# Kernel tuning notes

Hardware: AMD Instinct MI355X
Metric: run time of the kernel (lower is better)

Reference implementation:

```python
import jax, jax.numpy as jnp
import numpy as np

N, B, NPG, DEG, F = 16384, 128, 128, 8, 128
E = N * DEG
H1, C1, H2, C2, H3, C3 = 3, 128, 2, 64, 2, 32
D = H1 * C1 + H2 * C2 + C3  # 544
K = 30
ND = 2048
LAMDA = 0.8


def _gatv2(x, src, dst, Wl, Wr, att, b, h, c, concat):
    n = x.shape[0]
    xl = (x @ Wl).reshape(n, h, c)
    xr = (x @ Wr).reshape(n, h, c)
    e = jax.nn.leaky_relu(xl[src] + xr[dst], 0.2)           # [E+N, h, c]
    logit = jnp.einsum('ehc,hc->eh', e, att)
    m = jax.lax.stop_gradient(jax.ops.segment_max(logit, dst, num_segments=n))
    a = jnp.exp(logit - m[dst])
    z = jax.ops.segment_sum(a, dst, num_segments=n)
    a = a / z[dst]
    out = jax.ops.segment_sum(xl[src] * a[:, :, None], dst, num_segments=n)
    out = out.reshape(n, h * c) if concat else out.mean(axis=1)
    return out + b


def _bn(x, g, b):
    m = x.mean(0)
    v = ((x - m) ** 2).mean(0)
    return (x - m) * jax.lax.rsqrt(v + 1e-5) * g + b


def _neighbor(emb, adj, W, b, idx):
    h = emb @ W + b
    A = adj + jnp.eye(adj.shape[0], dtype=adj.dtype)
    d = jax.lax.rsqrt(A.sum(axis=1))
    h = (1.0 - LAMDA) * h + LAMDA * ((d[:, None] * A * d[None, :]) @ h)
    v = h[idx]
    return v / jnp.clip(jnp.linalg.norm(v, axis=1, keepdims=True), 1e-12)


def setup_inputs():
    key = jax.random.key(0)
    it = iter(jax.random.split(key, 48))
    def nrm(shape, s=0.05):
        return jax.random.normal(next(it), shape, jnp.float32) * s
    src = jnp.repeat(jnp.arange(N, dtype=jnp.int32), DEG)
    dst = (src // NPG) * NPG + jax.random.randint(next(it), (E,), 0, NPG, dtype=jnp.int32)
    batch = jnp.arange(N, dtype=jnp.int32) // NPG
    return dict(
        x=jax.random.normal(next(it), (N, F), jnp.float32),
        edge_src=src, edge_dst=dst, batch=batch,
        pairs1=jax.random.randint(next(it), (B,), 0, ND, dtype=jnp.int32),
        pairs2=jax.random.randint(next(it), (B,), 0, ND, dtype=jnp.int32),
        drug_adj=(jax.random.uniform(next(it), (ND, ND)) < 0.01).astype(jnp.float32),
        drug_emb=jax.random.normal(next(it), (ND, ND), jnp.float32) * 0.1,
        dis_adj=(jax.random.uniform(next(it), (ND, ND)) < 0.01).astype(jnp.float32),
        dis_emb=jax.random.normal(next(it), (ND, ND), jnp.float32) * 0.1,
        Wde=nrm((ND, 32)), bde=jnp.zeros((32,), jnp.float32),
        Wse=nrm((ND, 32)), bse=jnp.zeros((32,), jnp.float32),
        W1l=nrm((F, H1 * C1)), W1r=nrm((F, H1 * C1)), att1=nrm((H1, C1)), b1=jnp.zeros((H1 * C1,), jnp.float32),
        W2l=nrm((H1 * C1, H2 * C2)), W2r=nrm((H1 * C1, H2 * C2)), att2=nrm((H2, C2)), b2=jnp.zeros((H2 * C2,), jnp.float32),
        W3l=nrm((H2 * C2, H3 * C3)), W3r=nrm((H2 * C2, H3 * C3)), att3=nrm((H3, C3)), b3=jnp.zeros((C3,), jnp.float32),
        g1=jnp.ones((H1 * C1,), jnp.float32), be1=jnp.zeros((H1 * C1,), jnp.float32),
        g2=jnp.ones((H2 * C2,), jnp.float32), be2=jnp.zeros((H2 * C2,), jnp.float32),
        Ws=nrm((D, K)), bs=jnp.zeros((K,), jnp.float32),
        Wg=nrm((D, D)), bg=jnp.zeros((D,), jnp.float32),
        Wl1=nrm((D * K + 64, 128)), bl1=jnp.zeros((128,), jnp.float32),
        Wl2=nrm((128, 1)), bl2=jnp.zeros((1,), jnp.float32),
    )


def _forward(x, drug_adj, drug_emb, dis_adj, dis_emb, Wde, bde, Wse, bse,
             W1l, W1r, att1, b1, W2l, W2r, att2, b2, W3l, W3r, att3, b3,
             g1, be1, g2, be2, Ws, bs, Wg, bg, Wl1, bl1, Wl2, bl2,
             edge_src, edge_dst, batch, pairs1, pairs2):
    loop = jnp.arange(N, dtype=edge_src.dtype)  # GATv2 self loops
    src = jnp.concatenate([edge_src, loop])
    dst = jnp.concatenate([edge_dst, loop])
    x1 = _bn(jax.nn.relu(_gatv2(x, src, dst, W1l, W1r, att1, b1, H1, C1, True)), g1, be1)
    x2 = _bn(jax.nn.relu(_gatv2(x1, src, dst, W2l, W2r, att2, b2, H2, C2, True)), g2, be2)
    x3 = _gatv2(x2, src, dst, W3l, W3r, att3, b3, H3, C3, False)
    xc = jnp.concatenate([x1, x2, x3], axis=1)              # [N, D]
    xd = xc.reshape(B, NPG, D)                              # to_dense_batch (equal graphs)
    adj = jnp.zeros((B, NPG, NPG), xc.dtype).at[
        batch[edge_src], edge_src % NPG, edge_dst % NPG].add(1.0)
    s = jax.nn.softmax(xd @ Ws + bs, axis=-1)               # [B, NPG, K]
    xp = jnp.einsum('bnk,bnd->bkd', s, xd)                  # pooled features
    ap = jnp.einsum('bnk,bnm,bml->bkl', s, adj, s)          # pooled adjacency
    ap = ap.at[:, jnp.arange(K), jnp.arange(K)].set(1.0)    # DenseGCNConv add_loop
    dg = jax.lax.rsqrt(jnp.clip(ap.sum(-1), 1.0))
    apn = dg[:, :, None] * ap * dg[:, None, :]
    xg = jax.nn.relu(jnp.einsum('bkl,bld->bkd', apn, xp @ Wg) + bg)
    de = _neighbor(drug_emb, drug_adj, Wde, bde, pairs1)    # [B, 32]
    se = _neighbor(dis_emb, dis_adj, Wse, bse, pairs2)      # [B, 32]
    g = jnp.concatenate([de, xg.reshape(B, K * D), se], axis=-1)
    h = jax.nn.relu(g @ Wl1 + bl1)
    return (h @ Wl2 + bl2)[:, 0]


def reference(x, edge_src, edge_dst, batch, pairs1, pairs2, drug_adj, drug_emb, dis_adj, dis_emb,
              Wde, bde, Wse, bse, W1l, W1r, att1, b1, W2l, W2r, att2, b2, W3l, W3r, att3, b3,
              g1, be1, g2, be2, Ws, bs, Wg, bg, Wl1, bl1, Wl2, bl2):
    return _forward(x, drug_adj, drug_emb, dis_adj, dis_emb, Wde, bde, Wse, bse,
                    W1l, W1r, att1, b1, W2l, W2r, att2, b2, W3l, W3r, att3, b3,
                    g1, be1, g2, be2, Ws, bs, Wg, bg, Wl1, bl1, Wl2, bl2,
                    edge_src, edge_dst, batch, pairs1, pairs2)
```

## Files before the change

kernel.cpp:

```cpp
#include <hip/hip_runtime.h>
#include <math.h>

#define CDIV(a,b) (((a)+(b)-1)/(b))
#define HMIN(a,b) ((a)<(b)?(a):(b))
#define MAXD 48

typedef __attribute__((ext_vector_type(8))) short bf16x8;
typedef __attribute__((ext_vector_type(4))) float f32x4;

static __device__ inline short f2bf(float x){
  unsigned u = __float_as_uint(x);
  unsigned r = (u + 0x7fffu + ((u >> 16) & 1u)) >> 16;
  return (short)r;
}
static __device__ inline float bf2f(short s){
  return __uint_as_float(((unsigned)(unsigned short)s) << 16);
}

__global__ __launch_bounds__(256)
void transpose_bf16(const float* __restrict__ B, int K, int N, short* __restrict__ Bt)
{
  __shared__ float t[32][33];
  int k0 = blockIdx.x*32, n0 = blockIdx.y*32;
  int c = threadIdx.x & 31, r8 = threadIdx.x >> 5;
  for (int rr = r8; rr < 32; rr += 8) {
    int k = k0+rr, n = n0+c;
    t[rr][c] = (k < K && n < N) ? B[(size_t)k*N + n] : 0.f;
  }
  __syncthreads();
  for (int rr = r8; rr < 32; rr += 8) {
    int n = n0+rr, k = k0+c;
    if (n < N && k < K) Bt[(size_t)n*K + k] = f2bf(t[c][rr]);
  }
}

__global__ __launch_bounds__(256)
void gemm_mfma(const float* __restrict__ A, int lda,
               const short* __restrict__ Bt,
               float* __restrict__ C, int ldc,
               int M, int N, int K,
               const float* __restrict__ bias, int relu, int ksplit)
{
  __shared__ short As[128][40];
  __shared__ short Bs[128][40];
  const int k0 = blockIdx.z * ksplit;
  const int k1 = HMIN(k0 + ksplit, K);
  C += (size_t)blockIdx.z * (size_t)M * ldc;
  const int bm = blockIdx.x * 128, bn = blockIdx.y * 128;
  const int tid = threadIdx.x;
  const int sr = tid >> 1;
  const int sk = (tid & 1) * 16;
  const int wave = tid >> 6;
  const int wr = (wave >> 1) * 64, wc = (wave & 1) * 64;
  const int lane = tid & 63;
  const int lrow = lane & 15, lk = (lane >> 4) * 8;

  f32x4 acc[4][4];
  #pragma unroll
  for (int i=0;i<4;i++)
    #pragma unroll
    for (int j=0;j<4;j++) acc[i][j] = (f32x4){0.f,0.f,0.f,0.f};

  const bool bok = (bn + sr) < N;
  for (int kb = k0; kb < k1; kb += 32) {
    __syncthreads();
    {
      const float* ap = A + (size_t)(bm + sr)*lda + kb + sk;
      float4 v0 = *(const float4*)(ap+0);
      float4 v1 = *(const float4*)(ap+4);
      float4 v2 = *(const float4*)(ap+8);
      float4 v3 = *(const float4*)(ap+12);
      bf16x8 w0, w1;
      w0[0]=f2bf(v0.x); w0[1]=f2bf(v0.y); w0[2]=f2bf(v0.z); w0[3]=f2bf(v0.w);
      w0[4]=f2bf(v1.x); w0[5]=f2bf(v1.y); w0[6]=f2bf(v1.z); w0[7]=f2bf(v1.w);
      w1[0]=f2bf(v2.x); w1[1]=f2bf(v2.y); w1[2]=f2bf(v2.z); w1[3]=f2bf(v2.w);
      w1[4]=f2bf(v3.x); w1[5]=f2bf(v3.y); w1[6]=f2bf(v3.z); w1[7]=f2bf(v3.w);
      *(bf16x8*)&As[sr][sk]   = w0;
      *(bf16x8*)&As[sr][sk+8] = w1;
    }
    {
      bf16x8 u0 = (bf16x8){0,0,0,0,0,0,0,0}, u1 = u0;
      if (bok) {
        const short* bp = Bt + (size_t)(bn + sr)*K + kb + sk;
        u0 = *(const bf16x8*)(bp);
        u1 = *(const bf16x8*)(bp+8);
      }
      *(bf16x8*)&Bs[sr][sk]   = u0;
      *(bf16x8*)&Bs[sr][sk+8] = u1;
    }
    __syncthreads();
    bf16x8 af[4], bfr[4];
    #pragma unroll
    for (int f=0;f<4;f++) af[f]  = *(const bf16x8*)&As[wr + f*16 + lrow][lk];
    #pragma unroll
    for (int f=0;f<4;f++) bfr[f] = *(const bf16x8*)&Bs[wc + f*16 + lrow][lk];
    #pragma unroll
    for (int i=0;i<4;i++)
      #pragma unroll
      for (int j=0;j<4;j++)
        acc[i][j] = __builtin_amdgcn_mfma_f32_16x16x32_bf16(af[i], bfr[j], acc[i][j], 0, 0, 0);
  }
  const int erow = (lane >> 4) * 4;
  const int ecol = lane & 15;
  #pragma unroll
  for (int j=0;j<4;j++) {
    int gcol = bn + wc + j*16 + ecol;
    if (gcol >= N) continue;
    float bv = bias ? bias[gcol] : 0.f;
    #pragma unroll
    for (int i=0;i<4;i++) {
      int grow = bm + wr + i*16 + erow;
      #pragma unroll
      for (int r=0;r<4;r++) {
        float v = acc[i][j][r] + bv;
        if (relu) v = fmaxf(v, 0.f);
        C[(size_t)(grow + r)*ldc + gcol] = v;
      }
    }
  }
}

__global__ __launch_bounds__(256)
void skinny_gemm32(const float* __restrict__ A, int lda,
                   const float* __restrict__ B,
                   float* __restrict__ Cp, int M, int ksplit)
{
  const int m0 = blockIdx.x * 32;
  const int k0 = blockIdx.z * ksplit;
  __shared__ float As[32][68];
  __shared__ float Bs[64][36];
  float acc[4] = {0.f,0.f,0.f,0.f};
  const int r  = threadIdx.x >> 3;
  const int cg = (threadIdx.x & 7) * 4;
  for (int kb = k0; kb < k0 + ksplit; kb += 64) {
    {
      int rr = threadIdx.x >> 3, ko = (threadIdx.x & 7)*8;
      const float* ap = &A[(size_t)(m0+rr)*lda + kb + ko];
      *(float4*)&As[rr][ko]   = *(const float4*)ap;
      *(float4*)&As[rr][ko+4] = *(const float4*)(ap+4);
      int br = threadIdx.x >> 2, co = (threadIdx.x & 3)*8;
      const float* bp = &B[(size_t)(kb+br)*32 + co];
      *(float4*)&Bs[br][co]   = *(const float4*)bp;
      *(float4*)&Bs[br][co+4] = *(const float4*)(bp+4);
    }
    __syncthreads();
    #pragma unroll
    for (int kk=0; kk<64; kk+=4) {
      float4 a4 = *(const float4*)&As[r][kk];
      float4 b0 = *(const float4*)&Bs[kk  ][cg];
      float4 b1 = *(const float4*)&Bs[kk+1][cg];
      float4 b2 = *(const float4*)&Bs[kk+2][cg];
      float4 b3 = *(const float4*)&Bs[kk+3][cg];
      acc[0] += a4.x*b0.x + a4.y*b1.x + a4.z*b2.x + a4.w*b3.x;
      acc[1] += a4.x*b0.y + a4.y*b1.y + a4.z*b2.y + a4.w*b3.y;
      acc[2] += a4.x*b0.z + a4.y*b1.z + a4.z*b2.z + a4.w*b3.z;
      acc[3] += a4.x*b0.w + a4.y*b1.w + a4.z*b2.w + a4.w*b3.w;
    }
    __syncthreads();
  }
  float* cp = Cp + ((size_t)blockIdx.z*M + m0 + r)*32 + cg;
  *(float4*)cp = make_float4(acc[0],acc[1],acc[2],acc[3]);
}

__global__ void build_adj(const int* __restrict__ src, const int* __restrict__ dst,
                          int E, float* __restrict__ adj)
{
  int e = blockIdx.x*blockDim.x + threadIdx.x;
  if (e >= E) return;
  int s = src[e], d = dst[e];
  int g = s >> 7;
  atomicAdd(&adj[((size_t)g*128 + (s & 127))*128 + (d & 127)], 1.0f);
}

__global__ __launch_bounds__(1024)
void build_nbr(const int* __restrict__ dst, int epg, int shift,
               int* __restrict__ nbr, int* __restrict__ deg)
{
  __shared__ short ld[1024];
  const int g = blockIdx.x;
  for (int i = threadIdx.x; i < epg; i += 1024) ld[i] = (short)(dst[g*epg + i] & 127);
  __syncthreads();
  const int d   = threadIdx.x >> 3;
  const int seg = threadIdx.x & 7;
  const int spe = epg >> 3;
  const int i0 = seg*spe, i1 = i0 + spe;
  int cnt = 0;
  for (int i = i0; i < i1; ++i) cnt += (ld[i] == (short)d) ? 1 : 0;
  int pre = cnt;
  #pragma unroll
  for (int off=1; off<8; off<<=1) {
    int v = __shfl_up(pre, off, 8);
    if (seg >= off) pre += v;
  }
  const int base  = pre - cnt;
  const int total = __shfl(pre, 7, 8);
  if (seg == 7) deg[g*128 + d] = HMIN(total, MAXD);
  const int lbase = (g*128 + d)*MAXD;
  int w = base;
  for (int i = i0; i < i1; ++i) {
    if (ld[i] == (short)d) {
      if (w < MAXD) nbr[lbase + w] = i >> shift;
      ++w;
    }
  }
}

template<int C, int NL>
__global__ __launch_bounds__(512)
void gat_attn_sp(const float* __restrict__ XL, const float* __restrict__ XR, int ldx,
                 const float* __restrict__ att,
                 const int* __restrict__ nbr, const int* __restrict__ deg,
                 const float* __restrict__ bias, int bias_per_head,
                 float* __restrict__ out, int ldo)
{
  constexpr int SPAN = C / NL;
  constexpr int NG = 512 / NL;
  constexpr int PADC = C + 8;
  __shared__ short xls[128][PADC];
  __shared__ float A_lds[128];
  __shared__ float lgs[NG][MAXD+4];
  const int g = blockIdx.x, hh = blockIdx.y;
  const int d0 = blockIdx.z * 64;
  const int colbase = hh*C;
  const int tid = threadIdx.x;
  const int lane = tid & (NL-1);
  const int grp  = tid / NL;

  for (int idx = tid; idx < 128*C/4; idx += 512) {
    int r = idx / (C/4), q4 = idx % (C/4);
    float4 v = *(const float4*)&XL[(size_t)(g*128+r)*ldx + colbase + q4*4];
    short4 w;
    w.x = f2bf(v.x); w.y = f2bf(v.y); w.z = f2bf(v.z); w.w = f2bf(v.w);
    *(short4*)&xls[r][q4*4] = w;
  }
  float attv[SPAN];
  #pragma unroll
  for (int j=0;j<SPAN;j++) attv[j] = att[hh*C + lane*SPAN + j];
  __syncthreads();

  for (int s = grp; s < 128; s += NG) {
    float a = 0.f;
    #pragma unroll
    for (int j4=0;j4<SPAN;j4+=4) {
      short4 xv = *(const short4*)&xls[s][lane*SPAN + j4];
      a += attv[j4+0]*bf2f(xv.x) + attv[j4+1]*bf2f(xv.y)
         + attv[j4+2]*bf2f(xv.z) + attv[j4+3]*bf2f(xv.w);
    }
    #pragma unroll
    for (int t=1;t<NL;t<<=1) a += __shfl_xor(a, t, 64);
    if (lane == 0) A_lds[s] = a;
  }
  __syncthreads();

  for (int d = d0 + grp; d < d0 + 64; d += NG) {
    float xrv[SPAN];
    #pragma unroll
    for (int j=0;j<SPAN;j++) xrv[j] = XR[(size_t)(g*128+d)*ldx + colbase + lane*SPAN + j];
    float B = 0.f;
    #pragma unroll
    for (int j=0;j<SPAN;j++) B += attv[j]*xrv[j];
    #pragma unroll
    for (int t=1;t<NL;t<<=1) B += __shfl_xor(B, t, 64);
    const int dgn = deg[g*128+d];
    const int base = (g*128+d)*MAXD;
    float m = -1e30f;
    for (int i = 0; i <= dgn; ++i) {
      int s = (i < dgn) ? nbr[base+i] : d;
      float dot = 0.f;
      #pragma unroll
      for (int j4=0;j4<SPAN;j4+=4) {
        short4 xv = *(const short4*)&xls[s][lane*SPAN + j4];
        dot += attv[j4+0]*fabsf(bf2f(xv.x) + xrv[j4+0]);
        dot += attv[j4+1]*fabsf(bf2f(xv.y) + xrv[j4+1]);
        dot += attv[j4+2]*fabsf(bf2f(xv.z) + xrv[j4+2]);
        dot += attv[j4+3]*fabsf(bf2f(xv.w) + xrv[j4+3]);
      }
      #pragma unroll
      for (int t=1;t<NL;t<<=1) dot += __shfl_xor(dot, t, 64);
      float lg = 0.6f*(A_lds[s] + B) + 0.4f*dot;
      if (lane == 0) lgs[grp][i] = lg;
      m = fmaxf(m, lg);
    }
    float z = 0.f;
    for (int i = lane; i <= dgn; i += NL) z += __expf(lgs[grp][i] - m);
    #pragma unroll
    for (int t=1;t<NL;t<<=1) z += __shfl_xor(z, t, 64);
    const float zinv = 1.f / z;
    for (int i = lane; i <= dgn; i += NL) lgs[grp][i] = __expf(lgs[grp][i] - m) * zinv;
    float acc[SPAN];
    #pragma unroll
    for (int j=0;j<SPAN;j++) acc[j]=0.f;
    for (int i = 0; i <= dgn; ++i) {
      int s = (i < dgn) ? nbr[base+i] : d;
      float P = lgs[grp][i];
      #pragma unroll
      for (int j4=0;j4<SPAN;j4+=4) {
        short4 xv = *(const short4*)&xls[s][lane*SPAN + j4];
        acc[j4+0] += P*bf2f(xv.x); acc[j4+1] += P*bf2f(xv.y);
        acc[j4+2] += P*bf2f(xv.z); acc[j4+3] += P*bf2f(xv.w);
      }
    }
    float o[SPAN];
    #pragma unroll
    for (int j=0;j<SPAN;j++) {
      int cc = lane*SPAN + j;
      float bv = bias ? (bias_per_head ? bias[colbase+cc] : bias[cc]) : 0.f;
      o[j] = acc[j] + bv;
    }
    float* op = &out[(size_t)(g*128+d)*ldo + colbase + lane*SPAN];
    #pragma unroll
    for (int j4=0;j4<SPAN;j4+=4)
      *(float4*)&op[j4] = make_float4(o[j4],o[j4+1],o[j4+2],o[j4+3]);
  }
}

__global__ __launch_bounds__(256)
void bn_partial(const float* __restrict__ in, int HC,
                float* __restrict__ psum, float* __restrict__ psq)
{
  const int cg = blockIdx.x, rb = blockIdx.y;
  const int cl = threadIdx.x & 31;
  const int rl = threadIdx.x >> 5;
  const int col = cg*32 + cl;
  float s = 0.f, s2 = 0.f;
  for (int r = rb*512 + rl; r < (rb+1)*512; r += 8) {
    float v = fmaxf(in[(size_t)r*HC + col], 0.f);
    s += v; s2 += v*v;
  }
  __shared__ float ls[8][33], ls2[8][33];
  ls[rl][cl] = s; ls2[rl][cl] = s2;
  __syncthreads();
  if (threadIdx.x < 32) {
    float a=0.f, a2=0.f;
    for (int r=0;r<8;r++){ a += ls[r][threadIdx.x]; a2 += ls2[r][threadIdx.x]; }
    psum[rb*HC + cg*32 + threadIdx.x] = a;
    psq [rb*HC + cg*32 + threadIdx.x] = a2;
  }
}

__global__ void bn_finalize(const float* __restrict__ psum, const float* __restrict__ psq,
                            int HC, float* __restrict__ mv)
{
  int c = blockIdx.x*blockDim.x + threadIdx.x;
  if (c >= HC) return;
  float s=0.f, s2=0.f;
  for (int r=0;r<32;r++){ s += psum[r*HC+c]; s2 += psq[r*HC+c]; }
  float m = s * (1.f/16384.f);
  float v = s2 * (1.f/16384.f) - m*m;
  mv[c] = m; mv[HC+c] = v;
}

__global__ void bn_apply(const float* __restrict__ in, int HC,
                         const float* __restrict__ mv,
                         const float* __restrict__ gamma, const float* __restrict__ beta,
                         float* __restrict__ out, int ldo, int total)
{
  int i = blockIdx.x*blockDim.x + threadIdx.x;
  if (i >= total) return;
  int r = i / HC, c = i % HC;
  float v = fmaxf(in[i], 0.f);
  out[(size_t)r*ldo + c] = (v - mv[c]) * rsqrtf(mv[HC+c] + 1e-5f) * gamma[c] + beta[c];
}

__global__ void combine3(const float* __restrict__ raw, float* __restrict__ xc)
{
  int i = blockIdx.x*blockDim.x + threadIdx.x;
  if (i >= 16384*32) return;
  int r = i >> 5, c = i & 31;
  xc[(size_t)r*544 + 512 + c] = 0.5f*(raw[r*64 + c] + raw[r*64 + 32 + c]);
}

__global__ void softmax30(float* __restrict__ s, int M)
{
  int w = (blockIdx.x*blockDim.x + threadIdx.x) >> 5;
  int lane = threadIdx.x & 31;
  if (w >= M) return;
  float v = (lane < 30) ? s[(size_t)w*30 + lane] : -1e30f;
  float m = v;
  for (int t=16;t>0;t>>=1) m = fmaxf(m, __shfl_xor(m, t, 32));
  float e = (lane < 30) ? __expf(v - m) : 0.f;
  float z = e;
  for (int t=16;t>0;t>>=1) z += __shfl_xor(z, t, 32);
  if (lane < 30) s[(size_t)w*30 + lane] = e / z;
}

__global__ __launch_bounds__(256)
void xp_kernel(const float* __restrict__ s, const float* __restrict__ xc,
               float* __restrict__ xp)
{
  const int b = blockIdx.x;
  const int d = blockIdx.y*256 + threadIdx.x;
  __shared__ float sb[128][32];
  for (int idx = threadIdx.x; idx < 128*30; idx += 256) {
    int n = idx/30, k = idx%30;
    sb[n][k] = s[(size_t)(b*128+n)*30 + k];
  }
  __syncthreads();
  if (d >= 544) return;
  float acc[30];
  #pragma unroll
  for (int k=0;k<30;k++) acc[k]=0.f;
  const float* xcp = xc + (size_t)b*128*544 + d;
  for (int n=0;n<128;n++) {
    float xcv = xcp[(size_t)n*544];
    const float4* sp = (const float4*)&sb[n][0];
    #pragma unroll
    for (int q=0;q<7;q++) {
      float4 v = sp[q];
      acc[q*4+0] += v.x*xcv; acc[q*4+1] += v.y*xcv;
      acc[q*4+2] += v.z*xcv; acc[q*4+3] += v.w*xcv;
    }
    float2 v2 = *(const float2*)&sb[n][28];
    acc[28] += v2.x*xcv; acc[29] += v2.y*xcv;
  }
  #pragma unroll
  for (int k=0;k<30;k++) xp[((size_t)b*30+k)*544 + d] = acc[k];
}

__global__ __launch_bounds__(256)
void pool_adj_kernel(const float* __restrict__ adj, const float* __restrict__ s,
                     float* __restrict__ apn)
{
  const int b = blockIdx.x;
  __shared__ float sb[128][32];
  __shared__ float t1s[128][32];
  __shared__ float apb[30][31];
  __shared__ float dg[30];
  for (int idx = threadIdx.x; idx < 128*30; idx += 256) {
    int n = idx/30, k = idx%30;
    sb[n][k] = s[(size_t)(b*128+n)*30 + k];
  }
  __syncthreads();
  if (threadIdx.x < 128) {
    const int i = threadIdx.x;
    float acc[30];
    #pragma unroll
    for (int k=0;k<30;k++) acc[k]=0.f;
    const float* arow = adj + ((size_t)b*128 + i)*128;
    for (int j=0;j<128;j++) {
      float a = arow[j];
      const float4* sp = (const float4*)&sb[j][0];
      #pragma unroll
      for (int q=0;q<7;q++) {
        float4 v = sp[q];
        acc[q*4+0] += v.x*a; acc[q*4+1] += v.y*a;
        acc[q*4+2] += v.z*a; acc[q*4+3] += v.w*a;
      }
      float2 v2 = *(const float2*)&sb[j][28];
      acc[28] += v2.x*a; acc[29] += v2.y*a;
    }
    #pragma unroll
    for (int k=0;k<30;k++) t1s[i][k] = acc[k];
  }
  __syncthreads();
  for (int idx = threadIdx.x; idx < 900; idx += 256) {
    int k = idx/30, l = idx%30;
    float acc = 0.f;
    for (int n=0;n<128;n++) acc += sb[n][k]*t1s[n][l];
    apb[k][l] = (k == l) ? 1.f : acc;
  }
  __syncthreads();
  if (threadIdx.x < 30) {
    float ssum = 0.f;
    for (int l=0;l<30;l++) ssum += apb[threadIdx.x][l];
    dg[threadIdx.x] = rsqrtf(fmaxf(ssum, 1.f));
  }
  __syncthreads();
  for (int idx = threadIdx.x; idx < 900; idx += 256) {
    int k = idx/30, l = idx%30;
    apn[(size_t)b*900 + idx] = dg[k]*dg[l]*apb[k][l];
  }
}

__global__ __launch_bounds__(256)
void xg_kernel(const float* __restrict__ apn, const float* __restrict__ xpw,
               const float* __restrict__ bg, float* __restrict__ g)
{
  int b = blockIdx.x;
  __shared__ float a[30][31];
  for (int idx = threadIdx.x; idx < 900; idx += 256)
    a[idx/30][idx%30] = apn[(size_t)b*900 + idx];
  __syncthreads();
  for (int idx = threadIdx.x; idx < 30*544; idx += 256) {
    int k = idx / 544, d = idx % 544;
    float acc = 0.f;
    for (int l=0;l<30;l++) acc += a[k][l] * xpw[((size_t)b*30 + l)*544 + d];
    g[(size_t)b*16384 + 32 + k*544 + d] = fmaxf(acc + bg[d], 0.f);
  }
}

__global__ __launch_bounds__(256)
void rowsum_rsqrt(const float* __restrict__ A, int n, float* __restrict__ dinv)
{
  int r = blockIdx.x;
  float s = 0.f;
  for (int j = threadIdx.x; j < n; j += 256) s += A[(size_t)r*n + j];
  for (int m=32;m>0;m>>=1) s += __shfl_xor(s, m, 64);
  __shared__ float red[4];
  if ((threadIdx.x & 63) == 0) red[threadIdx.x >> 6] = s;
  __syncthreads();
  if (threadIdx.x == 0) dinv[r] = rsqrtf(red[0]+red[1]+red[2]+red[3] + 1.f);
}

__global__ void scale_rows(const float* __restrict__ h, const float* __restrict__ dinv,
                           float* __restrict__ hd, int total)
{
  int i = blockIdx.x*blockDim.x + threadIdx.x;
  if (i >= total) return;
  hd[i] = h[i] * dinv[i >> 5];
}

__global__ void combine_h2(const float* __restrict__ hW, const float* __restrict__ u,
                           const float* __restrict__ hd, const float* __restrict__ dinv,
                           float* __restrict__ h2, int total)
{
  int i = blockIdx.x*blockDim.x + threadIdx.x;
  if (i >= total) return;
  h2[i] = 0.2f*hW[i] + 0.8f*dinv[i >> 5]*(u[i] + hd[i]);
}

__global__ void gather_norm(const float* __restrict__ h2, const int* __restrict__ idx,
                            float* __restrict__ g, int goff)
{
  int t = blockIdx.x*blockDim.x + threadIdx.x;
  if (t >= 128*32) return;
  int b = t >> 5, c = t & 31;
  float v = h2[(size_t)idx[b]*32 + c];
  float ss = v*v;
  for (int m=1;m<32;m<<=1) ss += __shfl_xor(ss, m, 32);
  float nrm = fmaxf(sqrtf(ss), 1e-12f);
  g[(size_t)b*16384 + goff + c] = v / nrm;
}

__global__ void reduce_parts(const float* __restrict__ part, const float* __restrict__ bias,
                             float* __restrict__ outp, int total, int nz, int ldc, int relu)
{
  int i = blockIdx.x*blockDim.x + threadIdx.x;
  if (i >= total) return;
  float s = 0.f;
  for (int p=0;p<nz;p++) s += part[(size_t)p*total + i];
  if (bias) s += bias[i % ldc];
  if (relu) s = fmaxf(s, 0.f);
  outp[i] = s;
}

__global__ void final_out(const float* __restrict__ h, const float* __restrict__ Wl2,
                          const float* __restrict__ bl2, float* __restrict__ out)
{
  int m = threadIdx.x;
  if (m >= 128) return;
  float s = 0.f;
  for (int k=0;k<128;k++) s += h[m*128 + k] * Wl2[k];
  out[m] = s + bl2[0];
}

extern "C" void kernel_launch(void* const* d_in, const int* in_sizes, int n_in,
                              void* d_out, int out_size, void* d_ws, size_t ws_size,
                              hipStream_t stream)
{
  const float* x        = (const float*)d_in[0];
  const int*   edge_src = (const int*)d_in[1];
  const int*   edge_dst = (const int*)d_in[2];
  const int*   pairs1   = (const int*)d_in[4];
  const int*   pairs2   = (const int*)d_in[5];
  const float* drug_adj = (const float*)d_in[6];
  const float* drug_emb = (const float*)d_in[7];
  const float* dis_adj  = (const float*)d_in[8];
  const float* dis_emb  = (const float*)d_in[9];
  const float* Wde = (const float*)d_in[10];
  const float* bde = (const float*)d_in[11];
  const float* Wse = (const float*)d_in[12];
  const float* bse = (const float*)d_in[13];
  const float* W1l = (const float*)d_in[14];
  const float* W1r = (const float*)d_in[15];
  const float* att1= (const float*)d_in[16];
  const float* b1  = (const float*)d_in[17];
  const float* W2l = (const float*)d_in[18];
  const float* W2r = (const float*)d_in[19];
  const float* att2= (const float*)d_in[20];
  const float* b2  = (const float*)d_in[21];
  const float* W3l = (const float*)d_in[22];
  const float* W3r = (const float*)d_in[23];
  const float* att3= (const float*)d_in[24];
  const float* b3  = (const float*)d_in[25];
  const float* g1  = (const float*)d_in[26];
  const float* be1 = (const float*)d_in[27];
  const float* g2  = (const float*)d_in[28];
  const float* be2 = (const float*)d_in[29];
  const float* Wsm = (const float*)d_in[30];
  const float* bs  = (const float*)d_in[31];
  const float* Wg  = (const float*)d_in[32];
  const float* bg  = (const float*)d_in[33];
  const float* Wl1 = (const float*)d_in[34];
  const float* bl1 = (const float*)d_in[35];
  const float* Wl2 = (const float*)d_in[36];
  const float* bl2 = (const float*)d_in[37];
  float* out = (float*)d_out;

  const int E = in_sizes[1];
  const int epg = E >> 7;
  const int shift = 31 - __builtin_clz(epg >> 7);

  float* ws  = (float*)d_ws;
  float* adj = ws;
  int*   nbr = (int*)adj;
  int*   degb= nbr + 16384*MAXD;
  float* xc  = ws + 2097152;
  float* P   = ws + 11010048;
  float* XLR = P;
  float* RAW = P + 12582912;
  float* bnp = ws + 29884416;
  float* bnq = bnp + 12288;
  float* mv  = bnq + 12288;
  short* wT  = (short*)(mv + 1024);
  float* sbuf = P;
  float* xp   = P + 491520;
  float* apn  = P + 3187200;
  float* xpw  = P + 3302400;
  float* gbuf = P + 5391360;
  float* hWd  = P + 7488512;  float* hdd  = hWd + 65536;
  float* ud   = hdd + 65536;  float* h2d  = ud  + 65536;
  float* dinvd= h2d + 65536;
  float* hWs_ = dinvd + 2048; float* hds  = hWs_ + 65536;
  float* us   = hds + 65536;  float* h2s  = us  + 65536;
  float* dinvs= h2s + 65536;
  float* partials = dinvs + 2048;
  float* hfin = partials + 1048576;
  float* epart = hfin + 16384;
  short* wgT  = (short*)epart;
  short* wl1T = (short*)RAW;

  build_nbr<<<128, 1024, 0, stream>>>(edge_dst, epg, shift, nbr, degb);

  transpose_bf16<<<dim3(4,12), 256, 0, stream>>>(W1l, 128, 384, wT);
  transpose_bf16<<<dim3(4,12), 256, 0, stream>>>(W1r, 128, 384, wT + 384*128);
  gemm_mfma<<<dim3(128,6,1), 256, 0, stream>>>(x, 128, wT, XLR, 768, 16384, 768, 128, nullptr, 0, 128);
  gat_attn_sp<128,16><<<dim3(128,3,2), 512, 0, stream>>>(XLR, XLR + 384, 768, att1, nbr, degb, b1, 1, RAW, 384);
  bn_partial<<<dim3(12,32), 256, 0, stream>>>(RAW, 384, bnp, bnq);
  bn_finalize<<<2, 256, 0, stream>>>(bnp, bnq, 384, mv);
  bn_apply<<<CDIV(16384*384,256), 256, 0, stream>>>(RAW, 384, mv, g1, be1, xc, 544, 16384*384);

  transpose_bf16<<<dim3(12,4), 256, 0, stream>>>(W2l, 384, 128, wT);
  transpose_bf16<<<dim3(12,4), 256, 0, stream>>>(W2r, 384, 128, wT + 128*384);
  gemm_mfma<<<dim3(128,2,1), 256, 0, stream>>>(xc, 544, wT, XLR, 256, 16384, 256, 384, nullptr, 0, 384);
  gat_attn_sp<64,8><<<dim3(128,2,2), 512, 0, stream>>>(XLR, XLR + 128, 256, att2, nbr, degb, b2, 1, RAW, 128);
  bn_partial<<<dim3(4,32), 256, 0, stream>>>(RAW, 128, bnp, bnq);
  bn_finalize<<<1, 256, 0, stream>>>(bnp, bnq, 128, mv);
  bn_apply<<<CDIV(16384*128,256), 256, 0, stream>>>(RAW, 128, mv, g2, be2, xc + 384, 544, 16384*128);

  transpose_bf16<<<dim3(4,2), 256, 0, stream>>>(W3l, 128, 64, wT);
  transpose_bf16<<<dim3(4,2), 256, 0, stream>>>(W3r, 128, 64, wT + 64*128);
  gemm_mfma<<<dim3(128,1,1), 256, 0, stream>>>(xc + 384, 544, wT, XLR, 128, 16384, 128, 128, nullptr, 0, 128);
  gat_attn_sp<32,8><<<dim3(128,2,2), 512, 0, stream>>>(XLR, XLR + 64, 128, att3, nbr, degb, b3, 0, RAW, 64);
  combine3<<<CDIV(16384*32,256), 256, 0, stream>>>(RAW, xc);

  hipMemsetAsync(adj, 0, (size_t)2097152*4, stream);
  build_adj<<<CDIV(E,256), 256, 0, stream>>>(edge_src, edge_dst, E, adj);

  transpose_bf16<<<dim3(17,1), 256, 0, stream>>>(Wsm, 544, 30, wT);
  gemm_mfma<<<dim3(128,1,1), 256, 0, stream>>>(xc, 544, wT, sbuf, 30, 16384, 30, 544, bs, 0, 544);
  softmax30<<<CDIV(16384*32,256), 256, 0, stream>>>(sbuf, 16384);
  xp_kernel<<<dim3(128,3), 256, 0, stream>>>(sbuf, xc, xp);
  pool_adj_kernel<<<128, 256, 0, stream>>>(adj, sbuf, apn);
  transpose_bf16<<<dim3(17,17), 256, 0, stream>>>(Wg, 544, 544, wgT);
  gemm_mfma<<<dim3(30,5,1), 256, 0, stream>>>(xp, 544, wgT, xpw, 544, 3840, 544, 544, nullptr, 0, 544);
  xg_kernel<<<128, 256, 0, stream>>>(apn, xpw, bg, gbuf);

  skinny_gemm32<<<dim3(64,1,8), 256, 0, stream>>>(drug_emb, 2048, Wde, epart, 2048, 256);
  reduce_parts<<<CDIV(65536,256), 256, 0, stream>>>(epart, bde, hWd, 65536, 8, 32, 0);
  rowsum_rsqrt<<<2048, 256, 0, stream>>>(drug_adj, 2048, dinvd);
  scale_rows<<<CDIV(65536,256), 256, 0, stream>>>(hWd, dinvd, hdd, 65536);
  skinny_gemm32<<<dim3(64,1,8), 256, 0, stream>>>(drug_adj, 2048, hdd, epart, 2048, 256);
  reduce_parts<<<CDIV(65536,256), 256, 0, stream>>>(epart, nullptr, ud, 65536, 8, 32, 0);
  combine_h2<<<CDIV(65536,256), 256, 0, stream>>>(hWd, ud, hdd, dinvd, h2d, 65536);
  gather_norm<<<CDIV(4096,256), 256, 0, stream>>>(h2d, pairs1, gbuf, 0);

  skinny_gemm32<<<dim3(64,1,8), 256, 0, stream>>>(dis_emb, 2048, Wse, epart, 2048, 256);
  reduce_parts<<<CDIV(65536,256), 256, 0, stream>>>(epart, bse, hWs_, 65536, 8, 32, 0);
  rowsum_rsqrt<<<2048, 256, 0, stream>>>(dis_adj, 2048, dinvs);
  scale_rows<<<CDIV(65536,256), 256, 0, stream>>>(hWs_, dinvs, hds, 65536);
  skinny_gemm32<<<dim3(64,1,8), 256, 0, stream>>>(dis_adj, 2048, hds, epart, 2048, 256);
  reduce_parts<<<CDIV(65536,256), 256, 0, stream>>>(epart, nullptr, us, 65536, 8, 32, 0);
  combine_h2<<<CDIV(65536,256), 256, 0, stream>>>(hWs_, us, hds, dinvs, h2s, 65536);
  gather_norm<<<CDIV(4096,256), 256, 0, stream>>>(h2s, pairs2, gbuf, 16352);

  transpose_bf16<<<dim3(512,4), 256, 0, stream>>>(Wl1, 16384, 128, wl1T);
  gemm_mfma<<<dim3(1,1,32), 256, 0, stream>>>(gbuf, 16384, wl1T, partials, 128, 128, 128, 16384, nullptr, 0, 512);
  reduce_parts<<<CDIV(16384,256), 256, 0, stream>>>(partials, bl1, hfin, 16384, 32, 128, 1);
  final_out<<<1, 128, 0, stream>>>(hfin, Wl2, bl2, out);
}
```

Baseline: 505.6 us.

## Compute neighbor propagation only for gathered rows, merge transposes, keep XL in fp32 LDS

Replaces the full 2048x2048 adjacency-times-h propagation (scale, skinny GEMM, reduce, combine, gather) with one kernel that computes only the 128 rows selected by the pair indices, then normalizes them. Pairs of weight transposes are merged into single launches to cut launch count. The GAT attention kernel now stores XL in LDS as fp32 instead of bf16, which removes conversions but doubles LDS footprint and may lower occupancy.

```diff
diff --git a/kernel.cpp b/kernel.cpp
--- a/kernel.cpp
+++ b/kernel.cpp
@@ -13,15 +13,35 @@
   unsigned r = (u + 0x7fffu + ((u >> 16) & 1u)) >> 16;
   return (short)r;
 }
-static __device__ inline float bf2f(short s){
-  return __uint_as_float(((unsigned)(unsigned short)s) << 16);
-}
 
 __global__ __launch_bounds__(256)
 void transpose_bf16(const float* __restrict__ B, int K, int N, short* __restrict__ Bt)
 {
   __shared__ float t[32][33];
   int k0 = blockIdx.x*32, n0 = blockIdx.y*32;
+  int c = threadIdx.x & 31, r8 = threadIdx.x >> 5;
+  for (int rr = r8; rr < 32; rr += 8) {
+    int k = k0+rr, n = n0+c;
+    t[rr][c] = (k < K && n < N) ? B[(size_t)k*N + n] : 0.f;
+  }
+  __syncthreads();
+  for (int rr = r8; rr < 32; rr += 8) {
+    int n = n0+rr, k = k0+c;
+    if (n < N && k < K) Bt[(size_t)n*K + k] = f2bf(t[c][rr]);
+  }
+}
+
+__global__ __launch_bounds__(256)
+void transpose_bf16_2(const float* __restrict__ A0, int K0, int N0, short* __restrict__ D0,
+                      const float* __restrict__ A1, int K1, int N1, short* __restrict__ D1)
+{
+  const float* B; short* Bt; int K, N;
+  if (blockIdx.z == 0) { B=A0; Bt=D0; K=K0; N=N0; } else { B=A1; Bt=D1; K=K1; N=N1; }
+  int ntx = CDIV(K,32), nty = CDIV(N,32);
+  int tile = blockIdx.x;
+  if (tile >= ntx*nty) return;
+  int k0 = (tile % ntx)*32, n0 = (tile / ntx)*32;
+  __shared__ float t[32][33];
   int c = threadIdx.x & 31, r8 = threadIdx.x >> 5;
   for (int rr = r8; rr < 32; rr += 8) {
     int k = k0+rr, n = n0+c;
@@ -215,8 +235,8 @@
 {
   constexpr int SPAN = C / NL;
   constexpr int NG = 512 / NL;
-  constexpr int PADC = C + 8;
-  __shared__ short xls[128][PADC];
+  constexpr int PADC = C + 4;
+  __shared__ float xls[128][PADC];
   __shared__ float A_lds[128];
   __shared__ float lgs[NG][MAXD+4];
   const int g = blockIdx.x, hh = blockIdx.y;
@@ -226,12 +246,10 @@
   const int lane = tid & (NL-1);
   const int grp  = tid / NL;
 
-  for (int idx = tid; idx < 128*C/4; idx += 512) {
+  for (int idx = tid; idx < 128*(C/4); idx += 512) {
     int r = idx / (C/4), q4 = idx % (C/4);
-    float4 v = *(const float4*)&XL[(size_t)(g*128+r)*ldx + colbase + q4*4];
-    short4 w;
-    w.x = f2bf(v.x); w.y = f2bf(v.y); w.z = f2bf(v.z); w.w = f2bf(v.w);
-    *(short4*)&xls[r][q4*4] = w;
+    *(float4*)&xls[r][q4*4] =
+      *(const float4*)&XL[(size_t)(g*128+r)*ldx + colbase + q4*4];
   }
   float attv[SPAN];
   #pragma unroll
@@ -242,9 +260,8 @@
     float a = 0.f;
     #pragma unroll
     for (int j4=0;j4<SPAN;j4+=4) {
-      short4 xv = *(const short4*)&xls[s][lane*SPAN + j4];
-      a += attv[j4+0]*bf2f(xv.x) + attv[j4+1]*bf2f(xv.y)
-         + attv[j4+2]*bf2f(xv.z) + attv[j4+3]*bf2f(xv.w);
+      float4 xv = *(const float4*)&xls[s][lane*SPAN + j4];
+      a += attv[j4+0]*xv.x + attv[j4+1]*xv.y + attv[j4+2]*xv.z + attv[j4+3]*xv.w;
     }
     #pragma unroll
     for (int t=1;t<NL;t<<=1) a += __shfl_xor(a, t, 64);
@@ -255,7 +272,9 @@
   for (int d = d0 + grp; d < d0 + 64; d += NG) {
     float xrv[SPAN];
     #pragma unroll
-    for (int j=0;j<SPAN;j++) xrv[j] = XR[(size_t)(g*128+d)*ldx + colbase + lane*SPAN + j];
+    for (int j4=0;j4<SPAN;j4+=4)
+      *(float4*)&xrv[j4] =
+        *(const float4*)&XR[(size_t)(g*128+d)*ldx + colbase + lane*SPAN + j4];
     float B = 0.f;
     #pragma unroll
     for (int j=0;j<SPAN;j++) B += attv[j]*xrv[j];
@@ -269,11 +288,11 @@
       float dot = 0.f;
       #pragma unroll
       for (int j4=0;j4<SPAN;j4+=4) {
-        short4 xv = *(const short4*)&xls[s][lane*SPAN + j4];
-        dot += attv[j4+0]*fabsf(bf2f(xv.x) + xrv[j4+0]);
-        dot += attv[j4+1]*fabsf(bf2f(xv.y) + xrv[j4+1]);
-        dot += attv[j4+2]*fabsf(bf2f(xv.z) + xrv[j4+2]);
-        dot += attv[j4+3]*fabsf(bf2f(xv.w) + xrv[j4+3]);
+        float4 xv = *(const float4*)&xls[s][lane*SPAN + j4];
+        dot += attv[j4+0]*fabsf(xv.x + xrv[j4+0]);
+        dot += attv[j4+1]*fabsf(xv.y + xrv[j4+1]);
+        dot += attv[j4+2]*fabsf(xv.z + xrv[j4+2]);
+        dot += attv[j4+3]*fabsf(xv.w + xrv[j4+3]);
       }
       #pragma unroll
       for (int t=1;t<NL;t<<=1) dot += __shfl_xor(dot, t, 64);
@@ -295,9 +314,9 @@
       float P = lgs[grp][i];
       #pragma unroll
       for (int j4=0;j4<SPAN;j4+=4) {
-        short4 xv = *(const short4*)&xls[s][lane*SPAN + j4];
-        acc[j4+0] += P*bf2f(xv.x); acc[j4+1] += P*bf2f(xv.y);
-        acc[j4+2] += P*bf2f(xv.z); acc[j4+3] += P*bf2f(xv.w);
+        float4 xv = *(const float4*)&xls[s][lane*SPAN + j4];
+        acc[j4+0] += P*xv.x; acc[j4+1] += P*xv.y;
+        acc[j4+2] += P*xv.z; acc[j4+3] += P*xv.w;
       }
     }
     float o[SPAN];
@@ -502,34 +521,34 @@
   if (threadIdx.x == 0) dinv[r] = rsqrtf(red[0]+red[1]+red[2]+red[3] + 1.f);
 }
 
-__global__ void scale_rows(const float* __restrict__ h, const float* __restrict__ dinv,
-                           float* __restrict__ hd, int total)
-{
-  int i = blockIdx.x*blockDim.x + threadIdx.x;
-  if (i >= total) return;
-  hd[i] = h[i] * dinv[i >> 5];
-}
-
-__global__ void combine_h2(const float* __restrict__ hW, const float* __restrict__ u,
-                           const float* __restrict__ hd, const float* __restrict__ dinv,
-                           float* __restrict__ h2, int total)
-{
-  int i = blockIdx.x*blockDim.x + threadIdx.x;
-  if (i >= total) return;
-  h2[i] = 0.2f*hW[i] + 0.8f*dinv[i >> 5]*(u[i] + hd[i]);
-}
-
-__global__ void gather_norm(const float* __restrict__ h2, const int* __restrict__ idx,
-                            float* __restrict__ g, int goff)
-{
-  int t = blockIdx.x*blockDim.x + threadIdx.x;
-  if (t >= 128*32) return;
-  int b = t >> 5, c = t & 31;
-  float v = h2[(size_t)idx[b]*32 + c];
-  float ss = v*v;
-  for (int m=1;m<32;m<<=1) ss += __shfl_xor(ss, m, 32);
-  float nrm = fmaxf(sqrtf(ss), 1e-12f);
-  g[(size_t)b*16384 + goff + c] = v / nrm;
+__global__ __launch_bounds__(256)
+void embed_tail(const float* __restrict__ adjM, const float* __restrict__ hW,
+                const float* __restrict__ dinv, const int* __restrict__ idx,
+                float* __restrict__ g, int goff)
+{
+  const int b = blockIdx.x;
+  const int row = idx[b];
+  const int c  = threadIdx.x & 31;
+  const int jc = threadIdx.x >> 5;
+  float u = 0.f;
+  for (int j = jc; j < 2048; j += 8)
+    u += adjM[(size_t)row*2048 + j] * hW[j*32 + c] * dinv[j];
+  __shared__ float red[8][33];
+  red[jc][c] = u;
+  __syncthreads();
+  if (threadIdx.x < 32) {
+    float s = 0.f;
+    #pragma unroll
+    for (int r=0;r<8;r++) s += red[r][threadIdx.x];
+    float hw = hW[(size_t)row*32 + threadIdx.x];
+    float dv = dinv[row];
+    float h2 = 0.2f*hw + 0.8f*dv*(s + hw*dv);
+    float ss = h2*h2;
+    #pragma unroll
+    for (int m=1;m<32;m<<=1) ss += __shfl_xor(ss, m, 32);
+    float nrm = fmaxf(sqrtf(ss), 1e-12f);
+    g[(size_t)b*16384 + goff + threadIdx.x] = h2 / nrm;
+  }
 }
 
 __global__ void reduce_parts(const float* __restrict__ part, const float* __restrict__ bias,
@@ -618,12 +637,10 @@
   float* apn  = P + 3187200;
   float* xpw  = P + 3302400;
   float* gbuf = P + 5391360;
-  float* hWd  = P + 7488512;  float* hdd  = hWd + 65536;
-  float* ud   = hdd + 65536;  float* h2d  = ud  + 65536;
-  float* dinvd= h2d + 65536;
-  float* hWs_ = dinvd + 2048; float* hds  = hWs_ + 65536;
-  float* us   = hds + 65536;  float* h2s  = us  + 65536;
-  float* dinvs= h2s + 65536;
+  float* hWd  = P + 7488512;
+  float* dinvd= hWd + 65536;
+  float* hWs_ = dinvd + 2048;
+  float* dinvs= hWs_ + 65536;
   float* partials = dinvs + 2048;
   float* hfin = partials + 1048576;
   float* epart = hfin + 16384;
@@ -632,24 +649,24 @@
 
   build_nbr<<<128, 1024, 0, stream>>>(edge_dst, epg, shift, nbr, degb);
 
-  transpose_bf16<<<dim3(4,12), 256, 0, stream>>>(W1l, 128, 384, wT);
-  transpose_bf16<<<dim3(4,12), 256, 0, stream>>>(W1r, 128, 384, wT + 384*128);
+  transpose_bf16_2<<<dim3(48,1,2), 256, 0, stream>>>(W1l, 128, 384, wT,
+                                                     W1r, 128, 384, wT + 384*128);
   gemm_mfma<<<dim3(128,6,1), 256, 0, stream>>>(x, 128, wT, XLR, 768, 16384, 768, 128, nullptr, 0, 128);
   gat_attn_sp<128,16><<<dim3(128,3,2), 512, 0, stream>>>(XLR, XLR + 384, 768, att1, nbr, degb, b1, 1, RAW, 384);
   bn_partial<<<dim3(12,32), 256, 0, stream>>>(RAW, 384, bnp, bnq);
   bn_finalize<<<2, 256, 0, stream>>>(bnp, bnq, 384, mv);
   bn_apply<<<CDIV(16384*384,256), 256, 0, stream>>>(RAW, 384, mv, g1, be1, xc, 544, 16384*384);
 
-  transpose_bf16<<<dim3(12,4), 256, 0, stream>>>(W2l, 384, 128, wT);
-  transpose_bf16<<<dim3(12,4), 256, 0, stream>>>(W2r, 384, 128, wT + 128*384);
+  transpose_bf16_2<<<dim3(48,1,2), 256, 0, stream>>>(W2l, 384, 128, wT,
+                                                     W2r, 384, 128, wT + 128*384);
   gemm_mfma<<<dim3(128,2,1), 256, 0, stream>>>(xc, 544, wT, XLR, 256, 16384, 256, 384, nullptr, 0, 384);
   gat_attn_sp<64,8><<<dim3(128,2,2), 512, 0, stream>>>(XLR, XLR + 128, 256, att2, nbr, degb, b2, 1, RAW, 128);
   bn_partial<<<dim3(4,32), 256, 0, stream>>>(RAW, 128, bnp, bnq);
   bn_finalize<<<1, 256, 0, stream>>>(bnp, bnq, 128, mv);
   bn_apply<<<CDIV(16384*128,256), 256, 0, stream>>>(RAW, 128, mv, g2, be2, xc + 384, 544, 16384*128);
 
-  transpose_bf16<<<dim3(4,2), 256, 0, stream>>>(W3l, 128, 64, wT);
-  transpose_bf16<<<dim3(4,2), 256, 0, stream>>>(W3r, 128, 64, wT + 64*128);
+  transpose_bf16_2<<<dim3(8,1,2), 256, 0, stream>>>(W3l, 128, 64, wT,
+                                                    W3r, 128, 64, wT + 64*128);
   gemm_mfma<<<dim3(128,1,1), 256, 0, stream>>>(xc + 384, 544, wT, XLR, 128, 16384, 128, 128, nullptr, 0, 128);
   gat_attn_sp<32,8><<<dim3(128,2,2), 512, 0, stream>>>(XLR, XLR + 64, 128, att3, nbr, degb, b3, 0, RAW, 64);
   combine3<<<CDIV(16384*32,256), 256, 0, stream>>>(RAW, xc);
@@ -657,32 +674,24 @@
   hipMemsetAsync(adj, 0, (size_t)2097152*4, stream);
   build_adj<<<CDIV(E,256), 256, 0, stream>>>(edge_src, edge_dst, E, adj);
 
-  transpose_bf16<<<dim3(17,1), 256, 0, stream>>>(Wsm, 544, 30, wT);
+  transpose_bf16_2<<<dim3(289,1,2), 256, 0, stream>>>(Wsm, 544, 30, wT,
+                                                      Wg, 544, 544, wgT);
   gemm_mfma<<<dim3(128,1,1), 256, 0, stream>>>(xc, 544, wT, sbuf, 30, 16384, 30, 544, bs, 0, 544);
   softmax30<<<CDIV(16384*32,256), 256, 0, stream>>>(sbuf, 16384);
   xp_kernel<<<dim3(128,3), 256, 0, stream>>>(sbuf, xc, xp);
   pool_adj_kernel<<<128, 256, 0, stream>>>(adj, sbuf, apn);
-  transpose_bf16<<<dim3(17,17), 256, 0, stream>>>(Wg, 544, 544, wgT);
   gemm_mfma<<<dim3(30,5,1), 256, 0, stream>>>(xp, 544, wgT, xpw, 544, 3840, 544, 544, nullptr, 0, 544);
   xg_kernel<<<128, 256, 0, stream>>>(apn, xpw, bg, gbuf);
 
   skinny_gemm32<<<dim3(64,1,8), 256, 0, stream>>>(drug_emb, 2048, Wde, epart, 2048, 256);
   reduce_parts<<<CDIV(65536,256), 256, 0, stream>>>(epart, bde, hWd, 65536, 8, 32, 0);
   rowsum_rsqrt<<<2048, 256, 0, stream>>>(drug_adj, 2048, dinvd);
-  scale_rows<<<CDIV(65536,256), 256, 0, stream>>>(hWd, dinvd, hdd, 65536);
-  skinny_gemm32<<<dim3(64,1,8), 256, 0, stream>>>(drug_adj, 2048, hdd, epart, 2048, 256);
-  reduce_parts<<<CDIV(65536,256), 256, 0, stream>>>(epart, nullptr, ud, 65536, 8, 32, 0);
-  combine_h2<<<CDIV(65536,256), 256, 0, stream>>>(hWd, ud, hdd, dinvd, h2d, 65536);
-  gather_norm<<<CDIV(4096,256), 256, 0, stream>>>(h2d, pairs1, gbuf, 0);
+  embed_tail<<<128, 256, 0, stream>>>(drug_adj, hWd, dinvd, pairs1, gbuf, 0);
 
   skinny_gemm32<<<dim3(64,1,8), 256, 0, stream>>>(dis_emb, 2048, Wse, epart, 2048, 256);
   reduce_parts<<<CDIV(65536,256), 256, 0, stream>>>(epart, bse, hWs_, 65536, 8, 32, 0);
   rowsum_rsqrt<<<2048, 256, 0, stream>>>(dis_adj, 2048, dinvs);
-  scale_rows<<<CDIV(65536,256), 256, 0, stream>>>(hWs_, dinvs, hds, 65536);
-  skinny_gemm32<<<dim3(64,1,8), 256, 0, stream>>>(dis_adj, 2048, hds, epart, 2048, 256);
-  reduce_parts<<<CDIV(65536,256), 256, 0, stream>>>(epart, nullptr, us, 65536, 8, 32, 0);
-  combine_h2<<<CDIV(65536,256), 256, 0, stream>>>(hWs_, us, hds, dinvs, h2s, 65536);
-  gather_norm<<<CDIV(4096,256), 256, 0, stream>>>(h2s, pairs2, gbuf, 16352);
+  embed_tail<<<128, 256, 0, stream>>>(dis_adj, hWs_, dinvs, pairs2, gbuf, 16352);
 
   transpose_bf16<<<dim3(512,4), 256, 0, stream>>>(Wl1, 16384, 128, wl1T);
   gemm_mfma<<<dim3(1,1,32), 256, 0, stream>>>(gbuf, 16384, wl1T, partials, 128, 128, 128, 16384, nullptr, 0, 512);
```

Result: slower. 600.5 us (+18.8%).
